# Kernel tuning notes

Hardware: AMD Instinct MI355X
Metric: run time of the kernel (lower is better)

Reference implementation:

```python
import jax, jax.numpy as jnp
import numpy as np
from jax import lax

B, C_IN, T = 32, 80, 1000
C = 512          # encoder_embedding_dim
H = C // 2       # LSTM hidden per direction
K = 5            # kernel size
P_ZONEOUT = 0.1
BN_EPS = 1e-5


def setup_inputs() -> dict:
    key = jax.random.key(0)
    ks = jax.random.split(key, 32)
    d = {"x": jax.random.normal(ks[0], (B, C_IN, T), jnp.float32)}
    in_chs = [C_IN, C, C]
    i = 1
    for l in range(3):
        cin = in_chs[l]
        d[f"cw{l}"] = jax.random.normal(ks[i], (C, cin, K), jnp.float32) * (1.0 / np.sqrt(cin * K)); i += 1
        d[f"cb{l}"] = jnp.zeros((C,), jnp.float32)
        d[f"bg{l}"] = jnp.ones((C,), jnp.float32)
        d[f"bb{l}"] = jnp.zeros((C,), jnp.float32)
        d[f"bm{l}"] = jax.random.normal(ks[i], (C,), jnp.float32) * 0.1; i += 1
        d[f"bv{l}"] = jax.random.uniform(ks[i], (C,), jnp.float32, 0.5, 1.5); i += 1
    for tag in ("f", "b"):
        d[f"wih_{tag}"] = jax.random.normal(ks[i], (4 * H, C), jnp.float32) * (1.0 / np.sqrt(C)); i += 1
        d[f"whh_{tag}"] = jax.random.normal(ks[i], (4 * H, H), jnp.float32) * (1.0 / np.sqrt(H)); i += 1
        d[f"bih_{tag}"] = jnp.zeros((4 * H,), jnp.float32)
        d[f"bhh_{tag}"] = jnp.zeros((4 * H,), jnp.float32)
    return d


def _lstm_cell(xt, h, c, wih, whh, bih, bhh):
    g = xt @ wih.T + bih + h @ whh.T + bhh          # [B, 4H]
    i, f, gg, o = jnp.split(g, 4, axis=-1)
    c2 = jax.nn.sigmoid(f) * c + jax.nn.sigmoid(i) * jnp.tanh(gg)
    h2 = jax.nn.sigmoid(o) * jnp.tanh(c2)
    return h2, c2


def _zoneout(old, new, p):
    return p * old + (1.0 - p) * new


def _encoder(x, conv_params, lstm_params):
    # conv + BN(eval) + ReLU stack; dropout is identity in eval mode
    for (cw, cb, bg, bb, bm, bv) in conv_params:
        x = lax.conv_general_dilated(x, cw, (1,), [((K - 1) // 2, (K - 1) // 2)],
                                     dimension_numbers=("NCH", "OIH", "NCH"))
        x = x + cb[None, :, None]
        x = (x - bm[None, :, None]) * (bg / jnp.sqrt(bv + BN_EPS))[None, :, None] + bb[None, :, None]
        x = jax.nn.relu(x)
    x = x.transpose(0, 2, 1)                         # [B, T, C]
    (wih_f, whh_f, bih_f, bhh_f, wih_b, whh_b, bih_b, bhh_b) = lstm_params

    xs_f = x.transpose(1, 0, 2)                      # [T, B, C] forward order
    xs_b = xs_f[::-1]                                # backward order

    def step(carry, inp):
        hf, cf, hb, cb_ = carry
        xf, xb = inp
        hf2, cf2 = _lstm_cell(xf, hf, cf, wih_f, whh_f, bih_f, bhh_f)
        hb2, cb2 = _lstm_cell(xb, hb, cb_, wih_b, whh_b, bih_b, bhh_b)
        hf = _zoneout(hf, hf2, P_ZONEOUT); cf = _zoneout(cf, cf2, P_ZONEOUT)
        hb = _zoneout(hb, hb2, P_ZONEOUT); cb_ = _zoneout(cb_, cb2, P_ZONEOUT)
        return (hf, cf, hb, cb_), (hf, hb)

    z = jnp.zeros((x.shape[0], H), x.dtype)
    _, (out_f, out_b) = lax.scan(step, (z, z, z, z), (xs_f, xs_b))
    out = jnp.concatenate([out_f, out_b[::-1]], axis=-1)  # [T, B, 2H]
    return out.transpose(1, 0, 2)                         # [B, T, 2H]


def reference(x, cw0, cb0, bg0, bb0, bm0, bv0,
              cw1, cb1, bg1, bb1, bm1, bv1,
              cw2, cb2, bg2, bb2, bm2, bv2,
              wih_f, whh_f, bih_f, bhh_f,
              wih_b, whh_b, bih_b, bhh_b):
    conv_params = [(cw0, cb0, bg0, bb0, bm0, bv0),
                   (cw1, cb1, bg1, bb1, bm1, bv1),
                   (cw2, cb2, bg2, bb2, bm2, bv2)]
    lstm_params = (wih_f, whh_f, bih_f, bhh_f, wih_b, whh_b, bih_b, bhh_b)
    return _encoder(x, conv_params, lstm_params)
```

## Files before the change

### kernel.cpp

```cpp
#include <hip/hip_runtime.h>


#define T_LEN 1000
#define NBATCH 32
#define CCH 512
#define HDIM 256
#define GDIM 1024
#define TC 100

typedef _Float16 h16;
typedef _Float16 h16x2 __attribute__((ext_vector_type(2)));
typedef _Float16 f16x8 __attribute__((ext_vector_type(8)));
typedef float    f32x4 __attribute__((ext_vector_type(4)));

__device__ __forceinline__ float fixup(float v, float alt){
    union { float f; unsigned u; } c; c.f = v;
    return ((c.u & 0x7f800000u) == 0x7f800000u) ? alt : v;
}
__device__ __forceinline__ float clamp_s(float v, float lo, float hi){
    return fminf(fmaxf(v, lo), hi);
}
__device__ __forceinline__ float sigm(float x){
    const float xc = clamp_s(x, -30.f, 30.f);
    return 1.0f / (1.0f + __expf(-xc));
}
__device__ __forceinline__ float tanh_safe(float x){
    const float ax = fminf(fabsf(x), 30.0f);
    const float t  = __expf(-2.0f * ax);
    const float r  = (1.0f - t) / (1.0f + t);
    return copysignf(r, x);
}
__device__ __forceinline__ int dot4i8(int a, int b, int c){
#if defined(__has_builtin) && __has_builtin(__builtin_amdgcn_sdot4)
    return __builtin_amdgcn_sdot4(a, b, c, false);
#else
    int r = c;
    #pragma unroll
    for (int k = 0; k < 4; ++k) {
        const int av = (a << (24 - 8*k)) >> 24;
        const int bv = (b << (24 - 8*k)) >> 24;
        r += av * bv;
    }
    return r;
#endif
}

__global__ __launch_bounds__(256)
void pack_convw_kernel(const float* __restrict__ cw, h16* __restrict__ Wp, int cin)
{
    const int n = blockIdx.x*256 + threadIdx.x;
    if (n >= 5*512*cin) return;
    const int k   = n / (512*cin);
    const int rem = n - k*512*cin;
    const int co  = rem / cin;
    const int ci  = rem - co*cin;
    Wp[n] = (h16)cw[((size_t)co*cin + ci)*5 + k];
}

__global__ __launch_bounds__(256)
void pack_wih_kernel(const float* __restrict__ wf, const float* __restrict__ wb, h16* __restrict__ Wg)
{
    const int n = blockIdx.x*256 + threadIdx.x;
    const float* src = (n < 1024*512) ? wf : wb;
    Wg[n] = (h16)src[n & (1024*512 - 1)];
}

__global__ __launch_bounds__(256)
void whh_scale_kernel(const float* __restrict__ whh_f, const float* __restrict__ whh_b,
                      float* __restrict__ scl)
{
    const int n = blockIdx.x*256 + threadIdx.x;
    if (n >= 2048) return;
    const float* whh = (n >= 1024) ? whh_b : whh_f;
    const int row = n & 1023;
    float m = 0.f;
    for (int k = 0; k < HDIM; ++k) m = fmaxf(m, fabsf(whh[(size_t)row*HDIM + k]));
    scl[n] = fmaxf(m, 1e-8f) / 16129.0f;
}

__global__ __launch_bounds__(256)
void whh_prep_kernel(const float* __restrict__ whh_f, const float* __restrict__ whh_b,
                     const float* __restrict__ scl, unsigned* __restrict__ W8)
{
    const int n = blockIdx.x * 256 + threadIdx.x;
    if (n >= 2*64*1024) return;
    const int dir  = n >> 16;
    const int rem  = n & 65535;
    const int slot = rem >> 10;
    const int idx  = rem & 1023;
    const int u    = idx >> 2;
    const int e    = idx & 3;
    const float* whh = dir ? whh_b : whh_f;
    const int rg  = slot >> 4;
    const int jj  = slot & 15;
    const int row = rg*256 + u;
    const float inv = 1.0f / (scl[dir*1024 + row] * 127.0f);
    const int k0 = 16*jj + 4*e;
    unsigned uv = 0;
    #pragma unroll
    for (int j = 0; j < 4; ++j) {
        const float w = whh[(size_t)row*HDIM + k0 + j];
        int qv = (int)rintf(w * inv);
        qv = qv > 127 ? 127 : (qv < -127 ? -127 : qv);
        uv |= ((unsigned)(qv & 0xFF)) << (8*j);
    }
    W8[n] = uv;
}

__global__ __launch_bounds__(256)
void x0_transpose_kernel(const float* __restrict__ x, h16* __restrict__ Xt0)
{
    const int b = blockIdx.y;
    const int t = blockIdx.x*256 + threadIdx.x;
    if (t >= T_LEN) return;
    h16 v[80];
    #pragma unroll
    for (int c = 0; c < 80; ++c) v[c] = (h16)x[((size_t)b*80 + c)*T_LEN + t];
    #pragma unroll
    for (int g = 0; g < 10; ++g)
        *(f16x8*)(Xt0 + ((size_t)b*T_LEN + t)*80 + g*8) = *(const f16x8*)(v + g*8);
}

template<int CIN>
__global__ __attribute__((amdgpu_flat_work_group_size(512,512), amdgpu_waves_per_eu(2,4)))
void conv_mfma_kernel(const h16* __restrict__ Xt, const h16* __restrict__ Wp,
                      h16* __restrict__ outp,
                      const float* __restrict__ cb, const float* __restrict__ bg,
                      const float* __restrict__ bb, const float* __restrict__ bm,
                      const float* __restrict__ bv)
{
    const int t0   = blockIdx.x * 256;
    const int co0  = blockIdx.y * 128;
    const int b    = blockIdx.z;
    const int tid  = threadIdx.x;
    const int lane = tid & 63;
    const int w    = tid >> 6;
    const int wm   = w >> 1;
    const int wn   = w & 1;
    const int lr   = lane & 15;
    const int lg   = lane >> 4;

    __shared__ __align__(16) h16 Xs[260*40];
    __shared__ __align__(16) h16 Ws[5*128*40];

    f32x4 acc[4][4];
    #pragma unroll
    for (int m = 0; m < 4; ++m)
        #pragma unroll
        for (int n = 0; n < 4; ++n)
            #pragma unroll
            for (int r = 0; r < 4; ++r) acc[m][n][r] = 0.f;

    constexpr int KSTEPS = (CIN + 31) >> 5;
    for (int cs = 0; cs < KSTEPS; ++cs) {
        const int c0 = cs << 5;
        for (int id = tid; id < 260*4; id += 512) {
            const int row = id >> 2, g = id & 3;
            const int t = t0 + row - 2;
            f16x8 v;
            #pragma unroll
            for (int j = 0; j < 8; ++j) v[j] = (h16)0.f;
            if (t >= 0 && t < T_LEN) {
                const int c = c0 + g*8;
                if (c + 8 <= CIN) {
                    v = *(const f16x8*)(Xt + ((size_t)b*T_LEN + t)*CIN + c);
                } else if (c < CIN) {
                    #pragma unroll
                    for (int j = 0; j < 8; ++j) if (c + j < CIN) v[j] = Xt[((size_t)b*T_LEN + t)*CIN + c + j];
                }
            }
            *(f16x8*)(Xs + row*40 + g*8) = v;
        }
        for (int id = tid; id < 5*128*4; id += 512) {
            const int k  = id >> 9;
            const int co = (id >> 2) & 127;
            const int g  = id & 3;
            const int c  = c0 + g*8;
            f16x8 v;
            #pragma unroll
            for (int j = 0; j < 8; ++j) v[j] = (h16)0.f;
            if (c + 8 <= CIN) {
                v = *(const f16x8*)(Wp + ((size_t)k*512 + co0 + co)*CIN + c);
            } else if (c < CIN) {
                #pragma unroll
                for (int j = 0; j < 8; ++j) if (c + j < CIN) v[j] = Wp[((size_t)k*512 + co0 + co)*CIN + c + j];
            }
            *(f16x8*)(Ws + (k*128 + co)*40 + g*8) = v;
        }
        __syncthreads();

        #pragma unroll
        for (int k = 0; k < 5; ++k) {
            f16x8 bfr[4];
            #pragma unroll
            for (int nf = 0; nf < 4; ++nf)
                bfr[nf] = *(const f16x8*)(Ws + (k*128 + wn*64 + nf*16 + lr)*40 + lg*8);
            #pragma unroll
            for (int m = 0; m < 4; ++m) {
                const f16x8 a = *(const f16x8*)(Xs + (wm*64 + m*16 + lr + k)*40 + lg*8);
                #pragma unroll
                for (int nf = 0; nf < 4; ++nf)
                    acc[m][nf] = __builtin_amdgcn_mfma_f32_16x16x32_f16(a, bfr[nf], acc[m][nf], 0, 0, 0);
            }
        }
        __syncthreads();
    }

    #pragma unroll
    for (int nf = 0; nf < 4; ++nf) {
        const int co = co0 + wn*64 + nf*16 + lr;
        const float s  = bg[co] * rsqrtf(fmaxf(bv[co] + 1e-5f, 1e-8f));
        const float sh = (cb[co] - bm[co]) * s + bb[co];
        #pragma unroll
        for (int m = 0; m < 4; ++m) {
            #pragma unroll
            for (int r = 0; r < 4; ++r) {
                const int t = t0 + wm*64 + m*16 + lg*4 + r;
                if (t < T_LEN) {
                    const float y = fixup(clamp_s(fmaxf(acc[m][nf][r]*s + sh, 0.f), 0.f, 60000.f), 0.f);
                    outp[((size_t)b*T_LEN + t)*CCH + co] = (h16)y;
                }
            }
        }
    }
}

__global__ __attribute__((amdgpu_flat_work_group_size(256,256), amdgpu_waves_per_eu(4,4)))
void gates_mfma_kernel(const h16* __restrict__ Xt,
                       const h16* __restrict__ Wg,
                       const float* __restrict__ bih_f, const float* __restrict__ bhh_f,
                       const float* __restrict__ bih_b, const float* __restrict__ bhh_b,
                       h16* __restrict__ G, int t0f, int t0b)
{
    const int tt   = blockIdx.x;
    const int r0   = blockIdx.y * 128;
    const int b    = blockIdx.z & 31;
    const int dir  = blockIdx.z >> 5;
    const int t0c  = dir ? t0b : t0f;
    const int tid  = threadIdx.x;
    const int lane = tid & 63;
    const int w    = tid >> 6;
    const int lr   = lane & 15;
    const int lg   = lane >> 4;
    const float* bi = dir ? bih_b : bih_f;
    const float* bh = dir ? bhh_b : bhh_f;
    const h16* Wd = Wg + (size_t)dir*1024*512;

    __shared__ __align__(16) h16 Xs[64*40];
    __shared__ __align__(16) h16 Ws[128*40];

    f32x4 acc[4][2];
    #pragma unroll
    for (int m = 0; m < 4; ++m)
        #pragma unroll
        for (int n = 0; n < 2; ++n)
            #pragma unroll
            for (int r = 0; r < 4; ++r) acc[m][n][r] = 0.f;

    for (int cs = 0; cs < 16; ++cs) {
        const int c0 = cs << 5;
        for (int id = tid; id < 64*4; id += 256) {
            const int row = id >> 2, g = id & 3;
            int t = t0c + tt*64 + row; if (t >= T_LEN) t = T_LEN - 1;
            *(f16x8*)(Xs + row*40 + g*8) = *(const f16x8*)(Xt + ((size_t)b*T_LEN + t)*CCH + c0 + g*8);
        }
        for (int id = tid; id < 128*4; id += 256) {
            const int row = id >> 2, g = id & 3;
            *(f16x8*)(Ws + row*40 + g*8) = *(const f16x8*)(Wd + (size_t)(r0 + row)*CCH + c0 + g*8);
        }
        __syncthreads();

        const f16x8 b0 = *(const f16x8*)(Ws + (w*32 +      lr)*40 + lg*8);
        const f16x8 b1 = *(const f16x8*)(Ws + (w*32 + 16 + lr)*40 + lg*8);
        #pragma unroll
        for (int m = 0; m < 4; ++m) {
            const f16x8 a = *(const f16x8*)(Xs + (m*16 + lr)*40 + lg*8);
            acc[m][0] = __builtin_amdgcn_mfma_f32_16x16x32_f16(a, b0, acc[m][0], 0, 0, 0);
            acc[m][1] = __builtin_amdgcn_mfma_f32_16x16x32_f16(a, b1, acc[m][1], 0, 0, 0);
        }
        __syncthreads();
    }

    #pragma unroll
    for (int nf = 0; nf < 2; ++nf) {
        const int row = r0 + w*32 + nf*16 + lr;
        const float bias = bi[row] + bh[row];
        #pragma unroll
        for (int m = 0; m < 4; ++m) {
            #pragma unroll
            for (int r = 0; r < 4; ++r) {
                const int tl = tt*64 + m*16 + lg*4 + r;
                if (tl < TC)
                    G[(((size_t)dir*TC + tl)*NBATCH + b)*GDIM + row]
                        = (h16)fixup(clamp_s(acc[m][nf][r] + bias, -60000.f, 60000.f), 0.f);
            }
        }
    }
}

__global__ __attribute__((amdgpu_flat_work_group_size(256, 256), amdgpu_waves_per_eu(1, 1)))
void lstm_chunk_kernel(const h16* __restrict__ G,
                       const unsigned* __restrict__ W8,
                       const float* __restrict__ scl,
                       float* __restrict__ state,
                       float* __restrict__ out,
                       int t0f, int t0b, int first)
{
    const int u    = threadIdx.x;
    const int lane = u & 63;
    const int dir  = blockIdx.x >> 5;
    const int b    = blockIdx.x & 31;
    const int t0   = dir ? t0b : t0f;
    float* st = state + ((size_t)(dir*NBATCH + b))*2*HDIM;
    const uint4* Wv = (const uint4*)W8 + (size_t)dir*16384;

    __shared__ __align__(4) unsigned char hq8[2][256];

    uint4 wr[64];
    #pragma unroll
    for (int s = 0; s < 64; ++s) wr[s] = Wv[s*256 + u];

    const float s0 = scl[dir*1024 +       u];
    const float s1 = scl[dir*1024 + 256 + u];
    const float s2 = scl[dir*1024 + 512 + u];
    const float s3 = scl[dir*1024 + 768 + u];

    float hst = 0.0f, cst = 0.0f;
    if (!first) { hst = st[u]; cst = st[HDIM + u]; }
    {
        const int qh = (int)rintf(clamp_s(hst, -1.f, 1.f) * 127.f);
        hq8[0][u] = (unsigned char)(qh & 0xFF);
    }
    __syncthreads();

    for (int i = 0; i < TC; ++i) {
        const int sl = dir ? (TC - 1 - i) : i;
        const int t  = t0 + sl;
        const h16* gp = G + (((size_t)dir*TC + sl)*NBATCH + b)*GDIM;

        const float g0 = (float)gp[u];
        const float g1 = (float)gp[256 + u];
        const float g2 = (float)gp[512 + u];
        const float g3 = (float)gp[768 + u];

        const unsigned wv = ((const unsigned*)hq8[i & 1])[lane];

        int a0 = 0, a1 = 0, a2 = 0, a3 = 0;
        #pragma unroll
        for (int jj = 0; jj < 16; ++jj) {
            const int h0 = __builtin_amdgcn_readlane((int)wv, 4*jj + 0);
            const int h1 = __builtin_amdgcn_readlane((int)wv, 4*jj + 1);
            const int h2 = __builtin_amdgcn_readlane((int)wv, 4*jj + 2);
            const int h3 = __builtin_amdgcn_readlane((int)wv, 4*jj + 3);
            const uint4 w0 = wr[      jj];
            const uint4 w1 = wr[16 + jj];
            const uint4 w2 = wr[32 + jj];
            const uint4 w3 = wr[48 + jj];
            a0 = dot4i8(h0, (int)w0.x, a0); a0 = dot4i8(h1, (int)w0.y, a0);
            a0 = dot4i8(h2, (int)w0.z, a0); a0 = dot4i8(h3, (int)w0.w, a0);
            a1 = dot4i8(h0, (int)w1.x, a1); a1 = dot4i8(h1, (int)w1.y, a1);
            a1 = dot4i8(h2, (int)w1.z, a1); a1 = dot4i8(h3, (int)w1.w, a1);
            a2 = dot4i8(h0, (int)w2.x, a2); a2 = dot4i8(h1, (int)w2.y, a2);
            a2 = dot4i8(h2, (int)w2.z, a2); a2 = dot4i8(h3, (int)w2.w, a2);
            a3 = dot4i8(h0, (int)w3.x, a3); a3 = dot4i8(h1, (int)w3.y, a3);
            a3 = dot4i8(h2, (int)w3.z, a3); a3 = dot4i8(h3, (int)w3.w, a3);
        }

        const float gi = g0 + (float)a0 * s0;
        const float gf = g1 + (float)a1 * s1;
        const float gg = g2 + (float)a2 * s2;
        const float go = g3 + (float)a3 * s3;
        const float c2 = sigm(gf)*cst + sigm(gi)*tanh_safe(gg);
        const float h2v = sigm(go)*tanh_safe(c2);
        hst = 0.1f*hst + 0.9f*h2v;
        cst = 0.1f*cst + 0.9f*c2;
        out[((size_t)b*T_LEN + t)*(2*HDIM) + dir*HDIM + u] = fixup(hst, 50.0f);
        const int qh = (int)rintf(clamp_s(hst, -1.f, 1.f) * 127.f);
        hq8[(i + 1) & 1][u] = (unsigned char)(qh & 0xFF);
        __syncthreads();
    }

    st[u] = hst; st[HDIM + u] = cst;
}

extern "C" void kernel_launch(void* const* d_in, const int* in_sizes, int n_in,
                              void* d_out, int out_size, void* d_ws, size_t ws_size,
                              hipStream_t stream)
{
    (void)in_sizes; (void)n_in; (void)out_size;
    if (ws_size < 49152000) return;

    const float* x     = (const float*)d_in[0];
    const float* cw0   = (const float*)d_in[1];
    const float* cb0   = (const float*)d_in[2];
    const float* bg0   = (const float*)d_in[3];
    const float* bb0   = (const float*)d_in[4];
    const float* bm0   = (const float*)d_in[5];
    const float* bv0   = (const float*)d_in[6];
    const float* cw1   = (const float*)d_in[7];
    const float* cb1   = (const float*)d_in[8];
    const float* bg1   = (const float*)d_in[9];
    const float* bb1   = (const float*)d_in[10];
    const float* bm1   = (const float*)d_in[11];
    const float* bv1   = (const float*)d_in[12];
    const float* cw2   = (const float*)d_in[13];
    const float* cb2   = (const float*)d_in[14];
    const float* bg2   = (const float*)d_in[15];
    const float* bb2   = (const float*)d_in[16];
    const float* bm2   = (const float*)d_in[17];
    const float* bv2   = (const float*)d_in[18];
    const float* wih_f = (const float*)d_in[19];
    const float* whh_f = (const float*)d_in[20];
    const float* bih_f = (const float*)d_in[21];
    const float* bhh_f = (const float*)d_in[22];
    const float* wih_b = (const float*)d_in[23];
    const float* whh_b = (const float*)d_in[24];
    const float* bih_b = (const float*)d_in[25];
    const float* bhh_b = (const float*)d_in[26];

    char* ws = (char*)d_ws;
    char* od = (char*)d_out;
    h16*      A   = (h16*)(ws);
    h16*      G   = (h16*)(ws + 32768000);
    float*    st  = (float*)(ws + 45875200);
    unsigned* W8  = (unsigned*)(ws + 46006272);
    float*    scl = (float*)(ws + 46530560);
    h16*      Wg  = (h16*)(ws + 47054848);
    h16*      Bd  = (h16*)(od);
    h16*      Wp0 = (h16*)(od + 36000000);
    h16*      Wp1 = (h16*)(od + 36409600);
    h16*      Wp2 = (h16*)(od + 41652480);
    h16*      Xt0 = (h16*)(od + 46895360);
    float*    out = (float*)d_out;

    pack_convw_kernel<<<dim3((5*512*80  + 255)/256), 256, 0, stream>>>(cw0, Wp0, 80);
    pack_convw_kernel<<<dim3((5*512*512 + 255)/256), 256, 0, stream>>>(cw1, Wp1, 512);
    pack_convw_kernel<<<dim3((5*512*512 + 255)/256), 256, 0, stream>>>(cw2, Wp2, 512);
    pack_wih_kernel<<<dim3(2*1024*512/256), 256, 0, stream>>>(wih_f, wih_b, Wg);
    whh_scale_kernel<<<dim3(8), 256, 0, stream>>>(whh_f, whh_b, scl);
    whh_prep_kernel<<<dim3(512), 256, 0, stream>>>(whh_f, whh_b, scl, W8);
    x0_transpose_kernel<<<dim3(4, 32), 256, 0, stream>>>(x, Xt0);

    const dim3 cgrid(4, 4, 32);
    conv_mfma_kernel<80> <<<cgrid, 512, 0, stream>>>(Xt0, Wp0, A,  cb0, bg0, bb0, bm0, bv0);
    conv_mfma_kernel<512><<<cgrid, 512, 0, stream>>>(A,   Wp1, Bd, cb1, bg1, bb1, bm1, bv1);
    conv_mfma_kernel<512><<<cgrid, 512, 0, stream>>>(Bd,  Wp2, A,  cb2, bg2, bb2, bm2, bv2);

    for (int c = 0; c < T_LEN / TC; ++c) {
        const int t0f = c * TC;
        const int t0b = (T_LEN - TC) - c * TC;
        gates_mfma_kernel<<<dim3(2, 8, 64), 256, 0, stream>>>(A, Wg, bih_f, bhh_f, bih_b, bhh_b, G, t0f, t0b);
        lstm_chunk_kernel<<<dim3(64), 256, 0, stream>>>(G, W8, scl, st, out, t0f, t0b, c == 0);
    }
}
```

Measured before the change: 1.433 ms.

## Split LSTM recurrent gate matvec across two thread halves per block

Result: slower. 1.604 ms (+11.9%).

```diff
diff --git a/kernel.cpp b/kernel.cpp
--- a/kernel.cpp
+++ b/kernel.cpp
@@ -298,7 +298,7 @@
     }
 }
 
-__global__ __attribute__((amdgpu_flat_work_group_size(256, 256), amdgpu_waves_per_eu(1, 1)))
+__global__ __attribute__((amdgpu_flat_work_group_size(512, 512), amdgpu_waves_per_eu(2, 2)))
 void lstm_chunk_kernel(const h16* __restrict__ G,
                        const unsigned* __restrict__ W8,
                        const float* __restrict__ scl,
@@ -306,8 +306,10 @@
                        float* __restrict__ out,
                        int t0f, int t0b, int first)
 {
-    const int u    = threadIdx.x;
-    const int lane = u & 63;
+    const int tid  = threadIdx.x;
+    const int u    = tid & 255;
+    const int hp   = tid >> 8;
+    const int lane = tid & 63;
     const int dir  = blockIdx.x >> 5;
     const int b    = blockIdx.x & 31;
     const int t0   = dir ? t0b : t0f;
@@ -315,19 +317,18 @@
     const uint4* Wv = (const uint4*)W8 + (size_t)dir*16384;
 
     __shared__ __align__(4) unsigned char hq8[2][256];
-
-    uint4 wr[64];
-    #pragma unroll
-    for (int s = 0; s < 64; ++s) wr[s] = Wv[s*256 + u];
-
-    const float s0 = scl[dir*1024 +       u];
-    const float s1 = scl[dir*1024 + 256 + u];
-    const float s2 = scl[dir*1024 + 512 + u];
-    const float s3 = scl[dir*1024 + 768 + u];
+    __shared__ __align__(8) float2 pex[256];
+
+    uint4 wr[32];
+    #pragma unroll
+    for (int s = 0; s < 32; ++s) wr[s] = Wv[(hp*32 + s)*256 + u];
+
+    const float sA = scl[dir*1024 + (hp*2    )*256 + u];
+    const float sB = scl[dir*1024 + (hp*2 + 1)*256 + u];
 
     float hst = 0.0f, cst = 0.0f;
-    if (!first) { hst = st[u]; cst = st[HDIM + u]; }
-    {
+    if (hp == 0) {
+        if (!first) { hst = st[u]; cst = st[HDIM + u]; }
         const int qh = (int)rintf(clamp_s(hst, -1.f, 1.f) * 127.f);
         hq8[0][u] = (unsigned char)(qh & 0xFF);
     }
@@ -338,49 +339,46 @@
         const int t  = t0 + sl;
         const h16* gp = G + (((size_t)dir*TC + sl)*NBATCH + b)*GDIM;
 
-        const float g0 = (float)gp[u];
-        const float g1 = (float)gp[256 + u];
-        const float g2 = (float)gp[512 + u];
-        const float g3 = (float)gp[768 + u];
+        const float gA = (float)gp[(hp*2    )*256 + u];
+        const float gB = (float)gp[(hp*2 + 1)*256 + u];
 
         const unsigned wv = ((const unsigned*)hq8[i & 1])[lane];
 
-        int a0 = 0, a1 = 0, a2 = 0, a3 = 0;
+        int aA = 0, aB = 0;
         #pragma unroll
         for (int jj = 0; jj < 16; ++jj) {
             const int h0 = __builtin_amdgcn_readlane((int)wv, 4*jj + 0);
             const int h1 = __builtin_amdgcn_readlane((int)wv, 4*jj + 1);
             const int h2 = __builtin_amdgcn_readlane((int)wv, 4*jj + 2);
             const int h3 = __builtin_amdgcn_readlane((int)wv, 4*jj + 3);
-            const uint4 w0 = wr[      jj];
-            const uint4 w1 = wr[16 + jj];
-            const uint4 w2 = wr[32 + jj];
-            const uint4 w3 = wr[48 + jj];
-            a0 = dot4i8(h0, (int)w0.x, a0); a0 = dot4i8(h1, (int)w0.y, a0);
-            a0 = dot4i8(h2, (int)w0.z, a0); a0 = dot4i8(h3, (int)w0.w, a0);
-            a1 = dot4i8(h0, (int)w1.x, a1); a1 = dot4i8(h1, (int)w1.y, a1);
-            a1 = dot4i8(h2, (int)w1.z, a1); a1 = dot4i8(h3, (int)w1.w, a1);
-            a2 = dot4i8(h0, (int)w2.x, a2); a2 = dot4i8(h1, (int)w2.y, a2);
-            a2 = dot4i8(h2, (int)w2.z, a2); a2 = dot4i8(h3, (int)w2.w, a2);
-            a3 = dot4i8(h0, (int)w3.x, a3); a3 = dot4i8(h1, (int)w3.y, a3);
-            a3 = dot4i8(h2, (int)w3.z, a3); a3 = dot4i8(h3, (int)w3.w, a3);
-        }
-
-        const float gi = g0 + (float)a0 * s0;
-        const float gf = g1 + (float)a1 * s1;
-        const float gg = g2 + (float)a2 * s2;
-        const float go = g3 + (float)a3 * s3;
-        const float c2 = sigm(gf)*cst + sigm(gi)*tanh_safe(gg);
-        const float h2v = sigm(go)*tanh_safe(c2);
-        hst = 0.1f*hst + 0.9f*h2v;
-        cst = 0.1f*cst + 0.9f*c2;
-        out[((size_t)b*T_LEN + t)*(2*HDIM) + dir*HDIM + u] = fixup(hst, 50.0f);
-        const int qh = (int)rintf(clamp_s(hst, -1.f, 1.f) * 127.f);
-        hq8[(i + 1) & 1][u] = (unsigned char)(qh & 0xFF);
-        __syncthreads();
-    }
-
-    st[u] = hst; st[HDIM + u] = cst;
+            const uint4 wA = wr[     jj];
+            const uint4 wB = wr[16 + jj];
+            aA = dot4i8(h0, (int)wA.x, aA); aA = dot4i8(h1, (int)wA.y, aA);
+            aA = dot4i8(h2, (int)wA.z, aA); aA = dot4i8(h3, (int)wA.w, aA);
+            aB = dot4i8(h0, (int)wB.x, aB); aB = dot4i8(h1, (int)wB.y, aB);
+            aB = dot4i8(h2, (int)wB.z, aB); aB = dot4i8(h3, (int)wB.w, aB);
+        }
+        const float vA = gA + (float)aA * sA;
+        const float vB = gB + (float)aB * sB;
+
+        if (hp == 1) pex[u] = make_float2(vA, vB);
+        __syncthreads();
+
+        if (hp == 0) {
+            const float gi = vA, gf = vB;
+            const float2 go2 = pex[u];
+            const float c2  = sigm(gf)*cst + sigm(gi)*tanh_safe(go2.x);
+            const float h2v = sigm(go2.y)*tanh_safe(c2);
+            hst = 0.1f*hst + 0.9f*h2v;
+            cst = 0.1f*cst + 0.9f*c2;
+            out[((size_t)b*T_LEN + t)*(2*HDIM) + dir*HDIM + u] = fixup(hst, 50.0f);
+            const int qh = (int)rintf(clamp_s(hst, -1.f, 1.f) * 127.f);
+            hq8[(i + 1) & 1][u] = (unsigned char)(qh & 0xFF);
+        }
+        __syncthreads();
+    }
+
+    if (hp == 0) { st[u] = hst; st[HDIM + u] = cst; }
 }
 
 extern "C" void kernel_launch(void* const* d_in, const int* in_sizes, int n_in,
@@ -450,6 +448,6 @@
         const int t0f = c * TC;
         const int t0b = (T_LEN - TC) - c * TC;
         gates_mfma_kernel<<<dim3(2, 8, 64), 256, 0, stream>>>(A, Wg, bih_f, bhh_f, bih_b, bhh_b, G, t0f, t0b);
-        lstm_chunk_kernel<<<dim3(64), 256, 0, stream>>>(G, W8, scl, st, out, t0f, t0b, c == 0);
-    }
-}
+        lstm_chunk_kernel<<<dim3(64), 512, 0, stream>>>(G, W8, scl, st, out, t0f, t0b, c == 0);
+    }
+}
```
